# Performance work log

Hardware: AMD Instinct MI355X
Metric: run time of the kernel (lower is better)

Reference implementation:

```python
import jax, jax.numpy as jnp
import numpy as np

B, S, E, H, F, V = 4, 2048, 1024, 16, 4096, 32000
D = E // H  # head_dim = 64
LN_EPS = 1e-5


def layer_norm(x, g, b):
    mu = jnp.mean(x, axis=-1, keepdims=True)
    var = jnp.mean(jnp.square(x - mu), axis=-1, keepdims=True)
    return (x - mu) * jax.lax.rsqrt(var + LN_EPS) * g + b


def setup_inputs() -> dict:
    key = jax.random.key(0)
    ks = jax.random.split(key, 12)
    s = 0.02
    return {
        "input_ids": jax.random.randint(ks[0], (B, S), 0, V),
        "attention_mask": jnp.ones((B, S), dtype=jnp.int32),
        "emb_table": jax.random.normal(ks[1], (V, E), jnp.float32) * s,
        "Wq": jax.random.normal(ks[2], (E, E), jnp.float32) * s,
        "bq": jnp.zeros((E,), jnp.float32),
        "Wk": jax.random.normal(ks[3], (E, E), jnp.float32) * s,
        "bk": jnp.zeros((E,), jnp.float32),
        "Wv": jax.random.normal(ks[4], (E, E), jnp.float32) * s,
        "bv": jnp.zeros((E,), jnp.float32),
        "Wo": jax.random.normal(ks[5], (E, E), jnp.float32) * s,
        "bo": jnp.zeros((E,), jnp.float32),
        "ln_g": jnp.ones((E,), jnp.float32),
        "ln_b": jnp.zeros((E,), jnp.float32),
        "W1": jax.random.normal(ks[6], (E, F), jnp.float32) * s,
        "b1": jnp.zeros((F,), jnp.float32),
        "W2": jax.random.normal(ks[7], (F, E), jnp.float32) * s,
        "b2": jnp.zeros((E,), jnp.float32),
        "Wp": jax.random.normal(ks[8], (E, 3), jnp.float32) * s,
        "bp": jnp.zeros((3,), jnp.float32),
    }


def reference(input_ids, attention_mask, emb_table, Wq, bq, Wk, bk, Wv, bv,
              Wo, bo, ln_g, ln_b, W1, b1, W2, b2, Wp, bp):
    b, s = input_ids.shape
    x = emb_table[input_ids]                                  # [B,S,E]
    q = (x @ Wq + bq).reshape(b, s, H, D).transpose(0, 2, 1, 3)  # [B,H,S,D]
    k = (x @ Wk + bk).reshape(b, s, H, D).transpose(0, 2, 1, 3)
    v = (x @ Wv + bv).reshape(b, s, H, D).transpose(0, 2, 1, 3)
    scores = jnp.einsum('bhqd,bhkd->bhqk', q, k) / jnp.sqrt(jnp.float32(D))
    mask = attention_mask[:, None, None, :]                   # [B,1,1,S]
    scores = jnp.where(mask == 0, -jnp.inf, scores)
    attn = jax.nn.softmax(scores, axis=-1)
    ctx = jnp.einsum('bhqk,bhkd->bhqd', attn, v)              # [B,H,S,D]
    ctx = ctx.transpose(0, 2, 1, 3).reshape(b, s, E)
    ctx = ctx @ Wo + bo
    h = layer_norm(ctx + x, ln_g, ln_b)
    ff = jax.nn.gelu(h @ W1 + b1, approximate=False) @ W2 + b2
    logits = ff @ Wp + bp                                     # [B,S,3]
    return logits.mean(axis=1)                                # [B,3]
```

## Files before the change

kernel.cpp:

```cpp
#include <hip/hip_runtime.h>
#include <hip/hip_bf16.h>
#include <math.h>

#define BB 4
#define SS 2048
#define EE 1024
#define HH 16
#define DD 64
#define FF 4096

typedef unsigned short u16;
typedef unsigned int u32;
typedef __bf16 bf16x8 __attribute__((ext_vector_type(8)));
typedef float f32x4 __attribute__((ext_vector_type(4)));

static __device__ __forceinline__ float gelu_exact(float v){
  return 0.5f * v * (1.0f + erff(v * 0.70710678118654752f));
}

static __device__ __forceinline__ u16 f2bf(float f){
  union { float f; u32 u; } x; x.f = f;
  u32 r = x.u + 0x7FFFu + ((x.u >> 16) & 1u);
  return (u16)(r >> 16);
}
static __device__ __forceinline__ void unpack2(u32 u, float& lo, float& hi){
  union { u32 u; float f; } a, b;
  a.u = u << 16; b.u = u & 0xFFFF0000u;
  lo = a.f; hi = b.f;
}

#define GLOAD_LDS16(g, l) \
  __builtin_amdgcn_global_load_lds((const __attribute__((address_space(1))) void*)(g), \
      (__attribute__((address_space(3))) void*)(l), 16, 0, 0)

__global__ __launch_bounds__(256) void embed_kernel(const int* __restrict__ ids,
    const float* __restrict__ emb, float* __restrict__ xf, u16* __restrict__ xbf){
  int row = blockIdx.x;
  int id  = ids[row];
  float4 v = ((const float4*)(emb + (size_t)id * EE))[threadIdx.x];
  ((float4*)(xf + (size_t)row * EE))[threadIdx.x] = v;
  ushort4 u; u.x = f2bf(v.x); u.y = f2bf(v.y); u.z = f2bf(v.z); u.w = f2bf(v.w);
  ((ushort4*)(xbf + (size_t)row * EE))[threadIdx.x] = u;
}

__global__ __launch_bounds__(256) void transpose_bf16(const float* __restrict__ W,
    u16* __restrict__ WT, int K, int N){
  __shared__ float tile[32][33];
  int n0 = blockIdx.x * 32, k0 = blockIdx.y * 32;
  int tx = threadIdx.x & 31, ty = threadIdx.x >> 5;
  #pragma unroll
  for (int i = 0; i < 4; i++)
    tile[ty + 8*i][tx] = W[(size_t)(k0 + ty + 8*i) * N + n0 + tx];
  __syncthreads();
  #pragma unroll
  for (int i = 0; i < 4; i++)
    WT[(size_t)(n0 + ty + 8*i) * K + k0 + tx] = f2bf(tile[tx][ty + 8*i]);
}

template<int MODE>
__global__ __launch_bounds__(256) void gemm_mfma(const u16* __restrict__ A,
    const u16* __restrict__ WT, const float* __restrict__ bias,
    const float* __restrict__ biasB, const float* __restrict__ biasC,
    u16* __restrict__ C, float* __restrict__ gsum, int M, int N, int K){
  __shared__ __attribute__((aligned(16))) u16 As[128 * 32];
  __shared__ __attribute__((aligned(16))) u16 Bs[128 * 32];

  const int tid = threadIdx.x;
  const int l = tid & 63, w = tid >> 6;
  const int lm = l & 15, lq = l >> 4;
  const int wm = (w >> 1) * 64, wn = (w & 1) * 64;
  const int r0 = blockIdx.y * 128, c0 = blockIdx.x * 128;

  const int srow0 = w * 32 + (l >> 2);
  const int scol  = (l & 3) * 8;
  const u16* Ab = A  + (size_t)(r0 + srow0) * K + scol;
  const u16* Bb = WT + (size_t)(c0 + srow0) * K + scol;
  u16* AsBase0 = &As[(w * 2)     * 512];
  u16* AsBase1 = &As[(w * 2 + 1) * 512];
  u16* BsBase0 = &Bs[(w * 2)     * 512];
  u16* BsBase1 = &Bs[(w * 2 + 1) * 512];

  f32x4 acc[4][4];
  const f32x4 zero = {0.f, 0.f, 0.f, 0.f};
  #pragma unroll
  for (int mi = 0; mi < 4; mi++)
    #pragma unroll
    for (int ni = 0; ni < 4; ni++) acc[mi][ni] = zero;

  for (int k0 = 0; k0 < K; k0 += 32){
    GLOAD_LDS16(Ab + k0,                    AsBase0);
    GLOAD_LDS16(Ab + (size_t)16 * K + k0,   AsBase1);
    GLOAD_LDS16(Bb + k0,                    BsBase0);
    GLOAD_LDS16(Bb + (size_t)16 * K + k0,   BsBase1);
    __syncthreads();

    bf16x8 af[4], bf[4];
    #pragma unroll
    for (int mi = 0; mi < 4; mi++)
      af[mi] = *(const bf16x8*)&As[(wm + mi*16 + lm) * 32 + lq * 8];
    #pragma unroll
    for (int ni = 0; ni < 4; ni++)
      bf[ni] = *(const bf16x8*)&Bs[(wn + ni*16 + lm) * 32 + lq * 8];
    #pragma unroll
    for (int mi = 0; mi < 4; mi++)
      #pragma unroll
      for (int ni = 0; ni < 4; ni++)
        acc[mi][ni] = __builtin_amdgcn_mfma_f32_16x16x32_bf16(af[mi], bf[ni], acc[mi][ni], 0, 0, 0);
    __syncthreads();
  }

  if constexpr (MODE == 0){
    #pragma unroll
    for (int ni = 0; ni < 4; ni++){
      int col = c0 + wn + ni*16 + lm;
      float bcol = bias[col];
      #pragma unroll
      for (int mi = 0; mi < 4; mi++){
        #pragma unroll
        for (int r = 0; r < 4; r++){
          int row = r0 + wm + mi*16 + lq*4 + r;
          C[(size_t)row * N + col] = f2bf(acc[mi][ni][r] + bcol);
        }
      }
    }
  } else if constexpr (MODE == 2){
    #pragma unroll
    for (int ni = 0; ni < 4; ni++){
      int col3 = c0 + wn + ni*16 + lm;
      int sel  = col3 >> 10;
      int colm = col3 & 1023;
      const float* bp_ = (sel == 0) ? bias : ((sel == 1) ? biasB : biasC);
      float bcol = bp_[colm];
      u16* dst = C + (size_t)sel * ((size_t)M * N);
      #pragma unroll
      for (int mi = 0; mi < 4; mi++){
        #pragma unroll
        for (int r = 0; r < 4; r++){
          int row = r0 + wm + mi*16 + lq*4 + r;
          dst[(size_t)row * N + colm] = f2bf(acc[mi][ni][r] + bcol);
        }
      }
    }
  } else {
    const int batch = r0 >> 11;
    #pragma unroll
    for (int ni = 0; ni < 4; ni++){
      int col = c0 + wn + ni*16 + lm;
      float bcol = bias[col];
      float cs = 0.f;
      #pragma unroll
      for (int mi = 0; mi < 4; mi++)
        #pragma unroll
        for (int r = 0; r < 4; r++)
          cs += gelu_exact(acc[mi][ni][r] + bcol);
      cs += __shfl_xor(cs, 16, 64);
      cs += __shfl_xor(cs, 32, 64);
      if (lq == 0) atomicAdd(&gsum[(size_t)batch * N + col], cs);
    }
  }
}

__global__ __launch_bounds__(512) void attn_mfma(const u16* __restrict__ q,
    const u16* __restrict__ k, const u16* __restrict__ v,
    const int* __restrict__ mask, u16* __restrict__ ctx){
  const int bh = blockIdx.y, b = bh >> 4, h = bh & 15;
  const int q0 = blockIdx.x * 128;
  const int tid = threadIdx.x;
  const int w = tid >> 6, l = tid & 63, lm = l & 15, lq = l >> 4;

  __shared__ __attribute__((aligned(16))) u16 Kt[64 * 72];
  __shared__ __attribute__((aligned(16))) u16 Vt[64 * 72];
  __shared__ __attribute__((aligned(16))) u16 Pw[8][16 * 72];
  __shared__ float mb[64];

  const u16* qrow = q + (size_t)(b*SS + q0 + w*16 + lm) * EE + h*DD + lq*8;
  const bf16x8 aq0 = *(const bf16x8*)qrow;
  const bf16x8 aq1 = *(const bf16x8*)(qrow + 32);

  f32x4 occ[4];
  const f32x4 zero = {0.f,0.f,0.f,0.f};
  #pragma unroll
  for (int ni = 0; ni < 4; ni++) occ[ni] = zero;
  float l_part[4] = {0.f, 0.f, 0.f, 0.f};

  const int kkey = (tid & 255) >> 2, kchunk = tid & 3;
  const u16* kbase = k + (size_t)(b*SS + kkey) * EE + h*DD + kchunk*16;
  const int vkey = tid & 63, vd0 = ((tid >> 6) & 3) * 16;
  const u16* vbase = v + (size_t)(b*SS + vkey) * EE + h*DD + vd0;

  for (int t0 = 0; t0 < SS; t0 += 64){
    if (tid < 256){
      uint4 kv0 = *(const uint4*)(kbase + (size_t)t0 * EE);
      uint4 kv1 = *(const uint4*)(kbase + (size_t)t0 * EE + 8);
      *(uint4*)&Kt[kkey*72 + kchunk*16]     = kv0;
      *(uint4*)&Kt[kkey*72 + kchunk*16 + 8] = kv1;
      if (tid < 64) mb[tid] = (mask[b*SS + t0 + tid] != 0) ? 0.f : -1e30f;
    } else {
      union { uint4 u; u16 s[8]; } va, vb;
      va.u = *(const uint4*)(vbase + (size_t)t0 * EE);
      vb.u = *(const uint4*)(vbase + (size_t)t0 * EE + 8);
      #pragma unroll
      for (int i = 0; i < 8; i++){
        Vt[(vd0 + i)    *72 + vkey] = va.s[i];
        Vt[(vd0 + 8 + i)*72 + vkey] = vb.s[i];
      }
    }
    __syncthreads();

    f32x4 sc[4];
    #pragma unroll
    for (int ni = 0; ni < 4; ni++){
      bf16x8 b0 = *(const bf16x8*)&Kt[(ni*16 + lm)*72 + lq*8];
      bf16x8 b1 = *(const bf16x8*)&Kt[(ni*16 + lm)*72 + 32 + lq*8];
      sc[ni] = zero;
      sc[ni] = __builtin_amdgcn_mfma_f32_16x16x32_bf16(aq0, b0, sc[ni], 0, 0, 0);
      sc[ni] = __builtin_amdgcn_mfma_f32_16x16x32_bf16(aq1, b1, sc[ni], 0, 0, 0);
    }

    #pragma unroll
    for (int ni = 0; ni < 4; ni++){
      float mbias = mb[ni*16 + lm];
      #pragma unroll
      for (int r = 0; r < 4; r++){
        float s = fminf(fmaf(sc[ni][r], 0.125f, mbias), 60.f);
        float p = __expf(s);
        l_part[r] += p;
        Pw[w][(lq*4 + r)*72 + ni*16 + lm] = f2bf(p);
      }
    }
    bf16x8 ap0 = *(const bf16x8*)&Pw[w][lm*72 + lq*8];
    bf16x8 ap1 = *(const bf16x8*)&Pw[w][lm*72 + 32 + lq*8];

    #pragma unroll
    for (int ni = 0; ni < 4; ni++){
      bf16x8 b0 = *(const bf16x8*)&Vt[(ni*16 + lm)*72 + lq*8];
      bf16x8 b1 = *(const bf16x8*)&Vt[(ni*16 + lm)*72 + 32 + lq*8];
      occ[ni] = __builtin_amdgcn_mfma_f32_16x16x32_bf16(ap0, b0, occ[ni], 0, 0, 0);
      occ[ni] = __builtin_amdgcn_mfma_f32_16x16x32_bf16(ap1, b1, occ[ni], 0, 0, 0);
    }
    __syncthreads();
  }

  float inv[4];
  #pragma unroll
  for (int r = 0; r < 4; r++){
    float s = l_part[r];
    s += __shfl_xor(s, 1, 64);
    s += __shfl_xor(s, 2, 64);
    s += __shfl_xor(s, 4, 64);
    s += __shfl_xor(s, 8, 64);
    inv[r] = 1.f / s;
  }
  #pragma unroll
  for (int ni = 0; ni < 4; ni++){
    int col = h*DD + ni*16 + lm;
    #pragma unroll
    for (int r = 0; r < 4; r++){
      int row = q0 + w*16 + lq*4 + r;
      ctx[(size_t)(b*SS + row) * EE + col] = f2bf(occ[ni][r] * inv[r]);
    }
  }
}

__global__ __launch_bounds__(256) void ln_kernel(const u16* __restrict__ c2,
    const float* __restrict__ x, const float* __restrict__ g,
    const float* __restrict__ bta, u16* __restrict__ h){
  int row = blockIdx.x, tid = threadIdx.x;
  uint2 cu = ((const uint2*)(c2 + (size_t)row * EE))[tid];
  float c0,c1,c2f,c3;
  unpack2(cu.x, c0, c1); unpack2(cu.y, c2f, c3);
  float4 xv = ((const float4*)(x + (size_t)row * EE))[tid];
  float4 y = make_float4(c0+xv.x, c1+xv.y, c2f+xv.z, c3+xv.w);
  float s  = y.x + y.y + y.z + y.w;
  float ss = y.x*y.x + y.y*y.y + y.z*y.z + y.w*y.w;
  #pragma unroll
  for (int off=32; off; off>>=1){
    s  += __shfl_xor(s,  off, 64);
    ss += __shfl_xor(ss, off, 64);
  }
  __shared__ float rs[4], rss[4];
  int w = tid >> 6;
  if ((tid & 63) == 0){ rs[w] = s; rss[w] = ss; }
  __syncthreads();
  float tot  = rs[0]+rs[1]+rs[2]+rs[3];
  float tots = rss[0]+rss[1]+rss[2]+rss[3];
  float mu  = tot  * (1.f/EE);
  float var = tots * (1.f/EE) - mu*mu;
  float inv = rsqrtf(var + 1e-5f);
  float4 gv = ((const float4*)g)[tid];
  float4 bv = ((const float4*)bta)[tid];
  ushort4 ou;
  ou.x = f2bf((y.x-mu)*inv*gv.x + bv.x);
  ou.y = f2bf((y.y-mu)*inv*gv.y + bv.y);
  ou.z = f2bf((y.z-mu)*inv*gv.z + bv.z);
  ou.w = f2bf((y.w-mu)*inv*gv.w + bv.w);
  ((ushort4*)(h + (size_t)row * EE))[tid] = ou;
}

__global__ __launch_bounds__(256) void w2wp_kernel(const float* __restrict__ W2,
    const float* __restrict__ Wp, float* __restrict__ W2Wp){
  int f0 = blockIdx.x * 8;
  int tid = threadIdx.x;
  int e0 = tid * 4;
  float wp[4][3];
  #pragma unroll
  for (int t = 0; t < 4; t++)
    #pragma unroll
    for (int j = 0; j < 3; j++) wp[t][j] = Wp[(e0 + t)*3 + j];
  __shared__ float red[3][4];
  for (int i = 0; i < 8; i++){
    int f = f0 + i;
    float4 wv = ((const float4*)(W2 + (size_t)f * EE))[tid];
    float w4[4] = {wv.x, wv.y, wv.z, wv.w};
    float p[3] = {0.f, 0.f, 0.f};
    #pragma unroll
    for (int t = 0; t < 4; t++)
      #pragma unroll
      for (int j = 0; j < 3; j++) p[j] += w4[t] * wp[t][j];
    #pragma unroll
    for (int j = 0; j < 3; j++){
      float sj = p[j];
      #pragma unroll
      for (int off = 32; off; off >>= 1) sj += __shfl_xor(sj, off, 64);
      if ((tid & 63) == 0) red[j][tid >> 6] = sj;
    }
    __syncthreads();
    if (tid < 3) W2Wp[f*3 + tid] = red[tid][0] + red[tid][1] + red[tid][2] + red[tid][3];
    __syncthreads();
  }
}

__global__ __launch_bounds__(256) void out_final(const float* __restrict__ gsum,
    const float* __restrict__ W2Wp, const float* __restrict__ b2,
    const float* __restrict__ Wp, const float* __restrict__ bp, float* __restrict__ out){
  int tid = threadIdx.x;
  float part[4][3];
  #pragma unroll
  for (int b = 0; b < 4; b++)
    #pragma unroll
    for (int j = 0; j < 3; j++) part[b][j] = 0.f;
  for (int f = tid; f < FF; f += 256){
    float w0 = W2Wp[f*3], w1 = W2Wp[f*3+1], w2v = W2Wp[f*3+2];
    #pragma unroll
    for (int b = 0; b < 4; b++){
      float g = gsum[b*FF + f] * (1.f/SS);
      part[b][0] += g * w0; part[b][1] += g * w1; part[b][2] += g * w2v;
    }
  }
  float bb[3] = {0.f, 0.f, 0.f};
  for (int e = tid; e < EE; e += 256){
    float bv = b2[e];
    bb[0] += bv * Wp[e*3]; bb[1] += bv * Wp[e*3+1]; bb[2] += bv * Wp[e*3+2];
  }
  __shared__ float red[15][4];
  int lane = tid & 63, w = tid >> 6;
  #pragma unroll
  for (int b = 0; b < 4; b++)
    #pragma unroll
    for (int j = 0; j < 3; j++){
      float s = part[b][j];
      #pragma unroll
      for (int off = 32; off; off >>= 1) s += __shfl_xor(s, off, 64);
      if (lane == 0) red[b*3 + j][w] = s;
    }
  #pragma unroll
  for (int j = 0; j < 3; j++){
    float s = bb[j];
    #pragma unroll
    for (int off = 32; off; off >>= 1) s += __shfl_xor(s, off, 64);
    if (lane == 0) red[12 + j][w] = s;
  }
  __syncthreads();
  if (tid < 12){
    int j = tid % 3;
    float s  = red[tid][0] + red[tid][1] + red[tid][2] + red[tid][3];
    float bj = red[12+j][0] + red[12+j][1] + red[12+j][2] + red[12+j][3];
    out[tid] = s + bj + bp[j];
  }
}

extern "C" void kernel_launch(void* const* d_in, const int* in_sizes, int n_in,
                              void* d_out, int out_size, void* d_ws, size_t ws_size,
                              hipStream_t stream) {
  const int M = BB * SS;
  const int* ids  = (const int*)d_in[0];
  const int* mask = (const int*)d_in[1];
  const float* emb = (const float*)d_in[2];
  const float* Wq = (const float*)d_in[3];  const float* bq = (const float*)d_in[4];
  const float* Wk = (const float*)d_in[5];  const float* bk = (const float*)d_in[6];
  const float* Wv = (const float*)d_in[7];  const float* bv = (const float*)d_in[8];
  const float* Wo = (const float*)d_in[9];  const float* bo = (const float*)d_in[10];
  const float* lg = (const float*)d_in[11]; const float* lb = (const float*)d_in[12];
  const float* W1 = (const float*)d_in[13]; const float* b1 = (const float*)d_in[14];
  const float* W2 = (const float*)d_in[15]; const float* b2 = (const float*)d_in[16];
  const float* Wp = (const float*)d_in[17]; const float* bp = (const float*)d_in[18];

  char* base = (char*)d_ws;
  const size_t SLOTF = (size_t)M * EE;
  float* xf   = (float*)base;
  u16*  xbf   = (u16*)(base + SLOTF*4);
  u16*  qbf   = (u16*)(base + SLOTF*6);
  u16*  kbf   = (u16*)(base + SLOTF*8);
  u16*  vbf   = (u16*)(base + SLOTF*10);
  u16*  ctxbf = (u16*)(base + SLOTF*12);
  u16*  c2bf  = qbf;
  u16*  hbf   = kbf;
  u16*  WqT   = (u16*)(base + SLOTF*14);
  u16*  WkT   = WqT + (size_t)EE*EE;
  u16*  WvT   = WkT + (size_t)EE*EE;
  u16*  WoT   = WvT + (size_t)EE*EE;
  u16*  W1T   = WoT + (size_t)EE*EE;
  float* gsum = (float*)(W1T + (size_t)FF*EE);
  float* w2wp = gsum + BB*FF;

  hipMemsetAsync(gsum, 0, BB*FF*sizeof(float), stream);

  embed_kernel<<<M, 256, 0, stream>>>(ids, emb, xf, xbf);

  transpose_bf16<<<dim3(EE/32, EE/32), 256, 0, stream>>>(Wq, WqT, EE, EE);
  transpose_bf16<<<dim3(EE/32, EE/32), 256, 0, stream>>>(Wk, WkT, EE, EE);
  transpose_bf16<<<dim3(EE/32, EE/32), 256, 0, stream>>>(Wv, WvT, EE, EE);
  transpose_bf16<<<dim3(EE/32, EE/32), 256, 0, stream>>>(Wo, WoT, EE, EE);
  transpose_bf16<<<dim3(FF/32, EE/32), 256, 0, stream>>>(W1, W1T, EE, FF);
  w2wp_kernel<<<FF/8, 256, 0, stream>>>(W2, Wp, w2wp);

  gemm_mfma<2><<<dim3(3*EE/128, M/128), 256, 0, stream>>>(
      xbf, WqT, bq, bk, bv, qbf, nullptr, M, EE, EE);

  attn_mfma<<<dim3(SS/128, BB*HH), 512, 0, stream>>>(qbf, kbf, vbf, mask, ctxbf);

  gemm_mfma<0><<<dim3(EE/128, M/128), 256, 0, stream>>>(
      ctxbf, WoT, bo, nullptr, nullptr, c2bf, nullptr, M, EE, EE);

  ln_kernel<<<M, 256, 0, stream>>>(c2bf, xf, lg, lb, hbf);

  gemm_mfma<1><<<dim3(FF/128, M/128), 256, 0, stream>>>(
      hbf, W1T, b1, nullptr, nullptr, nullptr, gsum, M, FF, EE);

  out_final<<<1, 256, 0, stream>>>(gsum, w2wp, b2, Wp, bp, (float*)d_out);
}
```

Before: 646.5 us.

## Restructure attention to 4 waves with 32 query rows each and prefetch K/V

The attention kernel now runs 256 threads per block, with each wave handling two 16-row query groups so every K/V fragment read from LDS feeds two MFMAs. The next K/V tile and mask are prefetched into registers before the current tile is computed. The V transpose is written to LDS as packed 32-bit stores, and exp is replaced by exp2 with a folded scale. The five weight-transpose launches are merged into one prep_weights launch. The changes cut LDS traffic and launch overhead, but raise register pressure per wave.

```diff
diff --git a/kernel.cpp b/kernel.cpp
--- a/kernel.cpp
+++ b/kernel.cpp
@@ -43,10 +43,22 @@
   ((ushort4*)(xbf + (size_t)row * EE))[threadIdx.x] = u;
 }
 
-__global__ __launch_bounds__(256) void transpose_bf16(const float* __restrict__ W,
-    u16* __restrict__ WT, int K, int N){
+__global__ __launch_bounds__(256) void prep_weights(const float* __restrict__ Wq,
+    const float* __restrict__ Wk, const float* __restrict__ Wv,
+    const float* __restrict__ Wo, const float* __restrict__ W1, u16* __restrict__ WT){
   __shared__ float tile[32][33];
-  int n0 = blockIdx.x * 32, k0 = blockIdx.y * 32;
+  int bid = blockIdx.x;
+  const float* W; u16* dst; int N, n0, k0;
+  if (bid < 4096){
+    W = W1; dst = WT + (size_t)4 * EE * EE; N = FF;
+    n0 = (bid & 127) * 32; k0 = (bid >> 7) * 32;
+  } else {
+    int idx = bid - 4096;
+    int which = idx >> 10, t = idx & 1023;
+    W = (which == 0) ? Wq : (which == 1) ? Wk : (which == 2) ? Wv : Wo;
+    dst = WT + (size_t)which * EE * EE; N = EE;
+    n0 = (t & 31) * 32; k0 = (t >> 5) * 32;
+  }
   int tx = threadIdx.x & 31, ty = threadIdx.x >> 5;
   #pragma unroll
   for (int i = 0; i < 4; i++)
@@ -54,7 +66,7 @@
   __syncthreads();
   #pragma unroll
   for (int i = 0; i < 4; i++)
-    WT[(size_t)(n0 + ty + 8*i) * K + k0 + tx] = f2bf(tile[tx][ty + 8*i]);
+    dst[(size_t)(n0 + ty + 8*i) * EE + k0 + tx] = f2bf(tile[tx][ty + 8*i]);
 }
 
 template<int MODE>
@@ -160,7 +172,7 @@
   }
 }
 
-__global__ __launch_bounds__(512) void attn_mfma(const u16* __restrict__ q,
+__global__ __launch_bounds__(256, 4) void attn_mfma(const u16* __restrict__ q,
     const u16* __restrict__ k, const u16* __restrict__ v,
     const int* __restrict__ mask, u16* __restrict__ ctx){
   const int bh = blockIdx.y, b = bh >> 4, h = bh & 15;
@@ -170,94 +182,122 @@
 
   __shared__ __attribute__((aligned(16))) u16 Kt[64 * 72];
   __shared__ __attribute__((aligned(16))) u16 Vt[64 * 72];
-  __shared__ __attribute__((aligned(16))) u16 Pw[8][16 * 72];
+  __shared__ __attribute__((aligned(16))) u16 Pw[4][32 * 72];
   __shared__ float mb[64];
 
-  const u16* qrow = q + (size_t)(b*SS + q0 + w*16 + lm) * EE + h*DD + lq*8;
-  const bf16x8 aq0 = *(const bf16x8*)qrow;
-  const bf16x8 aq1 = *(const bf16x8*)(qrow + 32);
-
-  f32x4 occ[4];
+  bf16x8 aq[2][2];
+  #pragma unroll
+  for (int mg = 0; mg < 2; mg++){
+    const u16* qrow = q + (size_t)(b*SS + q0 + w*32 + mg*16 + lm) * EE + h*DD + lq*8;
+    aq[mg][0] = *(const bf16x8*)qrow;
+    aq[mg][1] = *(const bf16x8*)(qrow + 32);
+  }
+
+  f32x4 occ[2][4];
   const f32x4 zero = {0.f,0.f,0.f,0.f};
   #pragma unroll
-  for (int ni = 0; ni < 4; ni++) occ[ni] = zero;
-  float l_part[4] = {0.f, 0.f, 0.f, 0.f};
-
-  const int kkey = (tid & 255) >> 2, kchunk = tid & 3;
-  const u16* kbase = k + (size_t)(b*SS + kkey) * EE + h*DD + kchunk*16;
-  const int vkey = tid & 63, vd0 = ((tid >> 6) & 3) * 16;
-  const u16* vbase = v + (size_t)(b*SS + vkey) * EE + h*DD + vd0;
+  for (int mg = 0; mg < 2; mg++)
+    #pragma unroll
+    for (int ni = 0; ni < 4; ni++) occ[mg][ni] = zero;
+  float l_part[2][4] = {{0.f,0.f,0.f,0.f},{0.f,0.f,0.f,0.f}};
+
+  const int kkey = tid >> 2, kc16 = (tid & 3) * 16;
+  const u16* kbase = k + (size_t)(b*SS + kkey) * EE + h*DD + kc16;
+  const int kp = tid & 31, vd0 = (tid >> 5) * 8;
+  const u16* vbase0 = v + (size_t)(b*SS + 2*kp) * EE + h*DD + vd0;
+  const u16* vbase1 = vbase0 + EE;
+
+  uint4 kr0 = *(const uint4*)(kbase);
+  uint4 kr1 = *(const uint4*)(kbase + 8);
+  uint4 vr0 = *(const uint4*)(vbase0);
+  uint4 vr1 = *(const uint4*)(vbase1);
+  float mreg = 0.f;
+  if (tid < 64) mreg = (mask[b*SS + tid] != 0) ? 0.f : -1e30f;
+
+  const float SCALE_LOG2E = 0.125f * 1.4426950408889634f;
 
   for (int t0 = 0; t0 < SS; t0 += 64){
-    if (tid < 256){
-      uint4 kv0 = *(const uint4*)(kbase + (size_t)t0 * EE);
-      uint4 kv1 = *(const uint4*)(kbase + (size_t)t0 * EE + 8);
-      *(uint4*)&Kt[kkey*72 + kchunk*16]     = kv0;
-      *(uint4*)&Kt[kkey*72 + kchunk*16 + 8] = kv1;
-      if (tid < 64) mb[tid] = (mask[b*SS + t0 + tid] != 0) ? 0.f : -1e30f;
-    } else {
+    *(uint4*)&Kt[kkey*72 + kc16]     = kr0;
+    *(uint4*)&Kt[kkey*72 + kc16 + 8] = kr1;
+    {
       union { uint4 u; u16 s[8]; } va, vb;
-      va.u = *(const uint4*)(vbase + (size_t)t0 * EE);
-      vb.u = *(const uint4*)(vbase + (size_t)t0 * EE + 8);
+      va.u = vr0; vb.u = vr1;
       #pragma unroll
       for (int i = 0; i < 8; i++){
-        Vt[(vd0 + i)    *72 + vkey] = va.s[i];
-        Vt[(vd0 + 8 + i)*72 + vkey] = vb.s[i];
-      }
-    }
-    __syncthreads();
-
-    f32x4 sc[4];
+        u32 pk = (u32)va.s[i] | ((u32)vb.s[i] << 16);
+        *(u32*)&Vt[(vd0 + i)*72 + 2*kp] = pk;
+      }
+    }
+    if (tid < 64) mb[tid] = mreg;
+    __syncthreads();
+
+    if (t0 + 64 < SS){
+      kr0 = *(const uint4*)(kbase + (size_t)(t0 + 64) * EE);
+      kr1 = *(const uint4*)(kbase + (size_t)(t0 + 64) * EE + 8);
+      vr0 = *(const uint4*)(vbase0 + (size_t)(t0 + 64) * EE);
+      vr1 = *(const uint4*)(vbase1 + (size_t)(t0 + 64) * EE);
+      if (tid < 64) mreg = (mask[b*SS + t0 + 64 + tid] != 0) ? 0.f : -1e30f;
+    }
+
+    #pragma unroll
+    for (int mg = 0; mg < 2; mg++){
+      #pragma unroll
+      for (int ni = 0; ni < 4; ni++){
+        bf16x8 b0 = *(const bf16x8*)&Kt[(ni*16 + lm)*72 + lq*8];
+        bf16x8 b1 = *(const bf16x8*)&Kt[(ni*16 + lm)*72 + 32 + lq*8];
+        f32x4 sc = zero;
+        sc = __builtin_amdgcn_mfma_f32_16x16x32_bf16(aq[mg][0], b0, sc, 0, 0, 0);
+        sc = __builtin_amdgcn_mfma_f32_16x16x32_bf16(aq[mg][1], b1, sc, 0, 0, 0);
+        float mbias = mb[ni*16 + lm];
+        #pragma unroll
+        for (int r = 0; r < 4; r++){
+          float s = fminf(fmaf(sc[r], SCALE_LOG2E, mbias), 80.f);
+          float p = __builtin_amdgcn_exp2f(s);
+          l_part[mg][r] += p;
+          Pw[w][(mg*16 + lq*4 + r)*72 + ni*16 + lm] = f2bf(p);
+        }
+      }
+    }
+    bf16x8 ap[2][2];
+    #pragma unroll
+    for (int mg = 0; mg < 2; mg++){
+      ap[mg][0] = *(const bf16x8*)&Pw[w][(mg*16 + lm)*72 + lq*8];
+      ap[mg][1] = *(const bf16x8*)&Pw[w][(mg*16 + lm)*72 + 32 + lq*8];
+    }
+
     #pragma unroll
     for (int ni = 0; ni < 4; ni++){
-      bf16x8 b0 = *(const bf16x8*)&Kt[(ni*16 + lm)*72 + lq*8];
-      bf16x8 b1 = *(const bf16x8*)&Kt[(ni*16 + lm)*72 + 32 + lq*8];
-      sc[ni] = zero;
-      sc[ni] = __builtin_amdgcn_mfma_f32_16x16x32_bf16(aq0, b0, sc[ni], 0, 0, 0);
-      sc[ni] = __builtin_amdgcn_mfma_f32_16x16x32_bf16(aq1, b1, sc[ni], 0, 0, 0);
-    }
-
+      bf16x8 vb0 = *(const bf16x8*)&Vt[(ni*16 + lm)*72 + lq*8];
+      bf16x8 vb1 = *(const bf16x8*)&Vt[(ni*16 + lm)*72 + 32 + lq*8];
+      #pragma unroll
+      for (int mg = 0; mg < 2; mg++){
+        occ[mg][ni] = __builtin_amdgcn_mfma_f32_16x16x32_bf16(ap[mg][0], vb0, occ[mg][ni], 0, 0, 0);
+        occ[mg][ni] = __builtin_amdgcn_mfma_f32_16x16x32_bf16(ap[mg][1], vb1, occ[mg][ni], 0, 0, 0);
+      }
+    }
+    __syncthreads();
+  }
+
+  #pragma unroll
+  for (int mg = 0; mg < 2; mg++){
+    float inv[4];
+    #pragma unroll
+    for (int r = 0; r < 4; r++){
+      float s = l_part[mg][r];
+      s += __shfl_xor(s, 1, 64);
+      s += __shfl_xor(s, 2, 64);
+      s += __shfl_xor(s, 4, 64);
+      s += __shfl_xor(s, 8, 64);
+      inv[r] = 1.f / s;
+    }
     #pragma unroll
     for (int ni = 0; ni < 4; ni++){
-      float mbias = mb[ni*16 + lm];
+      int col = h*DD + ni*16 + lm;
       #pragma unroll
       for (int r = 0; r < 4; r++){
-        float s = fminf(fmaf(sc[ni][r], 0.125f, mbias), 60.f);
-        float p = __expf(s);
-        l_part[r] += p;
-        Pw[w][(lq*4 + r)*72 + ni*16 + lm] = f2bf(p);
-      }
-    }
-    bf16x8 ap0 = *(const bf16x8*)&Pw[w][lm*72 + lq*8];
-    bf16x8 ap1 = *(const bf16x8*)&Pw[w][lm*72 + 32 + lq*8];
-
-    #pragma unroll
-    for (int ni = 0; ni < 4; ni++){
-      bf16x8 b0 = *(const bf16x8*)&Vt[(ni*16 + lm)*72 + lq*8];
-      bf16x8 b1 = *(const bf16x8*)&Vt[(ni*16 + lm)*72 + 32 + lq*8];
-      occ[ni] = __builtin_amdgcn_mfma_f32_16x16x32_bf16(ap0, b0, occ[ni], 0, 0, 0);
-      occ[ni] = __builtin_amdgcn_mfma_f32_16x16x32_bf16(ap1, b1, occ[ni], 0, 0, 0);
-    }
-    __syncthreads();
-  }
-
-  float inv[4];
-  #pragma unroll
-  for (int r = 0; r < 4; r++){
-    float s = l_part[r];
-    s += __shfl_xor(s, 1, 64);
-    s += __shfl_xor(s, 2, 64);
-    s += __shfl_xor(s, 4, 64);
-    s += __shfl_xor(s, 8, 64);
-    inv[r] = 1.f / s;
-  }
-  #pragma unroll
-  for (int ni = 0; ni < 4; ni++){
-    int col = h*DD + ni*16 + lm;
-    #pragma unroll
-    for (int r = 0; r < 4; r++){
-      int row = q0 + w*16 + lq*4 + r;
-      ctx[(size_t)(b*SS + row) * EE + col] = f2bf(occ[ni][r] * inv[r]);
+        int row = q0 + w*32 + mg*16 + lq*4 + r;
+        ctx[(size_t)(b*SS + row) * EE + col] = f2bf(occ[mg][ni][r] * inv[r]);
+      }
     }
   }
 }
@@ -406,10 +446,7 @@
   u16*  c2bf  = qbf;
   u16*  hbf   = kbf;
   u16*  WqT   = (u16*)(base + SLOTF*14);
-  u16*  WkT   = WqT + (size_t)EE*EE;
-  u16*  WvT   = WkT + (size_t)EE*EE;
-  u16*  WoT   = WvT + (size_t)EE*EE;
-  u16*  W1T   = WoT + (size_t)EE*EE;
+  u16*  W1T   = WqT + (size_t)4*EE*EE;
   float* gsum = (float*)(W1T + (size_t)FF*EE);
   float* w2wp = gsum + BB*FF;
 
@@ -417,20 +454,16 @@
 
   embed_kernel<<<M, 256, 0, stream>>>(ids, emb, xf, xbf);
 
-  transpose_bf16<<<dim3(EE/32, EE/32), 256, 0, stream>>>(Wq, WqT, EE, EE);
-  transpose_bf16<<<dim3(EE/32, EE/32), 256, 0, stream>>>(Wk, WkT, EE, EE);
-  transpose_bf16<<<dim3(EE/32, EE/32), 256, 0, stream>>>(Wv, WvT, EE, EE);
-  transpose_bf16<<<dim3(EE/32, EE/32), 256, 0, stream>>>(Wo, WoT, EE, EE);
-  transpose_bf16<<<dim3(FF/32, EE/32), 256, 0, stream>>>(W1, W1T, EE, FF);
+  prep_weights<<<8192, 256, 0, stream>>>(Wq, Wk, Wv, Wo, W1, WqT);
   w2wp_kernel<<<FF/8, 256, 0, stream>>>(W2, Wp, w2wp);
 
   gemm_mfma<2><<<dim3(3*EE/128, M/128), 256, 0, stream>>>(
       xbf, WqT, bq, bk, bv, qbf, nullptr, M, EE, EE);
 
-  attn_mfma<<<dim3(SS/128, BB*HH), 512, 0, stream>>>(qbf, kbf, vbf, mask, ctxbf);
+  attn_mfma<<<dim3(SS/128, BB*HH), 256, 0, stream>>>(qbf, kbf, vbf, mask, ctxbf);
 
   gemm_mfma<0><<<dim3(EE/128, M/128), 256, 0, stream>>>(
-      ctxbf, WoT, bo, nullptr, nullptr, c2bf, nullptr, M, EE, EE);
+      ctxbf, WqT + (size_t)3*EE*EE, bo, nullptr, nullptr, c2bf, nullptr, M, EE, EE);
 
   ln_kernel<<<M, 256, 0, stream>>>(c2bf, xf, lg, lb, hbf);
 
```

Result: faster. 625.0 us (-3.3%).
